# Performance work log

Hardware: AMD Instinct MI355X
Metric: run time of the kernel (lower is better)

The kernel has to match this reference:

```python
import jax, jax.numpy as jnp
import numpy as np
from jax import lax

EPS = 1e-5
NEG_SLOPE = 0.1
RES_SCALE = float(np.sqrt(0.5))


def upsample2x(x):
    # bilinear, align_corners=False (half-pixel), matches torch nn.Upsample(mode='bilinear')
    B, C, H, W = x.shape
    return jax.image.resize(x, (B, C, 2 * H, 2 * W), method='bilinear')


def modulated_conv2d(x, weight, styles, eps=EPS):
    # x: [B, I, H, W]; weight: [O, I, kh, kw]; styles: [B, I]
    B, I, H, W = x.shape
    O, _, kh, kw = weight.shape
    wmod = weight[None] * styles[:, None, :, None, None]            # [B,O,I,kh,kw]
    demod = lax.rsqrt(jnp.sum(wmod * wmod, axis=(2, 3, 4)) + eps)   # [B,O]
    wmod = wmod * demod[:, :, None, None, None]
    x_g = x.reshape(1, B * I, H, W)
    w_g = wmod.reshape(B * O, I, kh, kw)
    out = lax.conv_general_dilated(
        x_g, w_g, window_strides=(1, 1), padding=[(1, 1), (1, 1)],
        feature_group_count=B,
        dimension_numbers=('NCHW', 'OIHW', 'NCHW'))
    return out.reshape(B, O, H, W)


def style_block(x, w, n, conv_w, A_w, A_b, B_w, B_b, upsample):
    if upsample:
        x = upsample2x(x)
    scores = w @ A_w.T + A_b                      # [B, in_ch]
    x = modulated_conv2d(x, conv_w, scores)
    noise = n @ B_w.T + B_b                        # [B, out_ch]
    x = x + noise[:, :, None, None]
    return jnp.where(x >= 0, x, NEG_SLOPE * x)     # LeakyReLU(0.1)


def setup_inputs() -> dict:
    key = jax.random.key(0)
    ks = jax.random.split(key, 16)
    Bn, Ci, Co, Wd, Nd, H = 8, 256, 128, 512, 512, 64
    s = lambda k, shape, scale=0.05: jax.random.normal(k, shape, jnp.float32) * scale
    return {
        'x': jax.random.normal(ks[0], (Bn, Ci, H, H), jnp.float32),
        'w': jax.random.normal(ks[1], (Bn, Wd), jnp.float32),
        'n': jax.random.normal(ks[2], (Bn, Nd), jnp.float32),
        'rgb': jax.random.normal(ks[3], (Bn, 3, H, H), jnp.float32),
        'conv1_w': s(ks[4], (Ci, Ci, 3, 3)),
        'A1_w': s(ks[5], (Ci, Wd)), 'A1_b': jnp.ones((Ci,), jnp.float32),
        'B1_w': s(ks[6], (Ci, Nd)), 'B1_b': jnp.zeros((Ci,), jnp.float32),
        'conv2_w': s(ks[7], (Co, Ci, 3, 3)),
        'A2_w': s(ks[8], (Ci, Wd)), 'A2_b': jnp.ones((Ci,), jnp.float32),
        'B2_w': s(ks[9], (Co, Nd)), 'B2_b': jnp.zeros((Co,), jnp.float32),
        'rgb_w': s(ks[10], (3, Co, 1, 1)),
        'rgb_b': jnp.zeros((3,), jnp.float32),
    }


def reference(x, w, n, rgb, conv1_w, A1_w, A1_b, B1_w, B1_b,
              conv2_w, A2_w, A2_b, B2_w, B2_b, rgb_w, rgb_b):
    x = style_block(x, w, n, conv1_w, A1_w, A1_b, B1_w, B1_b, upsample=False)
    x = style_block(x, w, n, conv2_w, A2_w, A2_b, B2_w, B2_b, upsample=True)
    to_rgb = lax.conv_general_dilated(
        x, rgb_w, (1, 1), padding=[(0, 0), (0, 0)],
        dimension_numbers=('NCHW', 'OIHW', 'NCHW')) + rgb_b[None, :, None, None]
    rgb_out = (to_rgb + upsample2x(rgb)) * RES_SCALE
    return x, rgb_out
```

## Files before the change

### kernel.cpp

```cpp
#include <hip/hip_runtime.h>
#include <math.h>

#define BN 8
#define C1 256
#define C2 128
#define WD 512

typedef float  f32x4  __attribute__((ext_vector_type(4)));
typedef short  bf16x8 __attribute__((ext_vector_type(8)));
typedef unsigned short ushort_t;
typedef ushort_t us8 __attribute__((ext_vector_type(8)));
typedef ushort_t us4 __attribute__((ext_vector_type(4)));

__device__ __forceinline__ int clampi(int v, int lo, int hi) {
    return v < lo ? lo : (v > hi ? hi : v);
}
__device__ __forceinline__ float bf2f(ushort_t u) {
    return __uint_as_float(((unsigned int)u) << 16);
}
__device__ __forceinline__ ushort_t f2bf(float f) {
    unsigned int u = __float_as_uint(f);
    u = (u + 0x7fff + ((u >> 16) & 1)) >> 16;
    return (ushort_t)u;
}

__global__ __launch_bounds__(256)
void affine_kernel(const float* __restrict__ w, const float* __restrict__ n,
                   const float* __restrict__ A1w, const float* __restrict__ A1b,
                   const float* __restrict__ B1w, const float* __restrict__ B1b,
                   const float* __restrict__ A2w, const float* __restrict__ A2b,
                   const float* __restrict__ B2w, const float* __restrict__ B2b,
                   float* __restrict__ s1, float* __restrict__ s2,
                   float* __restrict__ n1, float* __restrict__ n2) {
    int tid = threadIdx.x;
    int gw = blockIdx.x * 4 + (tid >> 6);
    int lane = tid & 63;
    if (gw >= BN * 896) return;
    int b = gw / 896;
    int j = gw % 896;
    const float* vec; const float* M; const float* bias; float* out; int o;
    if (j < 256)      { o = j;       vec = w + b * WD; M = A1w; bias = A1b; out = s1 + b * 256; }
    else if (j < 512) { o = j - 256; vec = w + b * WD; M = A2w; bias = A2b; out = s2 + b * 256; }
    else if (j < 768) { o = j - 512; vec = n + b * WD; M = B1w; bias = B1b; out = n1 + b * 256; }
    else              { o = j - 768; vec = n + b * WD; M = B2w; bias = B2b; out = n2 + b * 128; }
    const float* row = M + (size_t)o * WD;
    int k0 = lane * 8;
    float4 v0 = *(const float4*)(vec + k0), v1 = *(const float4*)(vec + k0 + 4);
    float4 r0 = *(const float4*)(row + k0), r1 = *(const float4*)(row + k0 + 4);
    float acc = v0.x*r0.x + v0.y*r0.y + v0.z*r0.z + v0.w*r0.w
              + v1.x*r1.x + v1.y*r1.y + v1.z*r1.z + v1.w*r1.w;
    #pragma unroll
    for (int m = 1; m < 64; m <<= 1) acc += __shfl_xor(acc, m, 64);
    if (lane == 0) out[o] = acc + bias[o];
}

__global__ __launch_bounds__(256)
void demod_kernel(const float* __restrict__ cw1, const float* __restrict__ cw2,
                  const float* __restrict__ s1, const float* __restrict__ s2,
                  float* __restrict__ d1, float* __restrict__ d2) {
    int tid = threadIdx.x;
    int gw = blockIdx.x * 4 + (tid >> 6);
    int lane = tid & 63;
    if (gw >= BN * 384) return;
    int b = gw / 384;
    int j = gw % 384;
    const float* wbase; const float* s; float* dout; int o;
    if (j < 256) { o = j;       wbase = cw1; s = s1 + b * 256; dout = d1 + b * 256; }
    else         { o = j - 256; wbase = cw2; s = s2 + b * 256; dout = d2 + b * 128; }
    float acc = 0.f;
    #pragma unroll
    for (int i = 0; i < 4; i++) {
        int ic = lane * 4 + i;
        float sv = s[ic]; sv *= sv;
        const float* wk = wbase + ((size_t)o * 256 + ic) * 9;
        float t = 0.f;
        #pragma unroll
        for (int k = 0; k < 9; k++) t += wk[k] * wk[k];
        acc += t * sv;
    }
    #pragma unroll
    for (int m = 1; m < 64; m <<= 1) acc += __shfl_xor(acc, m, 64);
    if (lane == 0) dout[o] = rsqrtf(acc + 1e-5f);
}

__global__ __launch_bounds__(256)
void wprep_kernel(const float* __restrict__ cw1, const float* __restrict__ cw2,
                  ushort_t* __restrict__ wT1, ushort_t* __restrict__ wT2) {
    int idx = blockIdx.x * 256 + threadIdx.x;
    if (idx < 256 * 256) {
        int oc = idx >> 8, ic = idx & 255;
        int kc = ic >> 5, icw = ic & 31;
        const float* src = cw1 + ((size_t)(oc * 256 + ic)) * 9;
        #pragma unroll
        for (int tap = 0; tap < 9; tap++)
            wT1[((size_t)((kc * 9 + tap) * 256 + oc)) * 32 + icw] = f2bf(src[tap]);
    } else if (idx < 256 * 256 + 128 * 256) {
        int e = idx - 256 * 256;
        int oc = e >> 8, ic = e & 255;
        int kc = ic >> 5, icw = ic & 31;
        const float* src = cw2 + ((size_t)(oc * 256 + ic)) * 9;
        #pragma unroll
        for (int tap = 0; tap < 9; tap++)
            wT2[((size_t)((kc * 9 + tap) * 128 + oc)) * 32 + icw] = f2bf(src[tap]);
    }
}

__global__ __launch_bounds__(256)
void xprep_kernel(const float* __restrict__ x, const float* __restrict__ s1,
                  ushort_t* __restrict__ xTp) {
    __shared__ ushort_t tile[64 * 264];
    int b = blockIdx.y;
    int px0 = blockIdx.x * 64;
    int t = threadIdx.x;
    int pxl = (t & 15) * 4;
    int icb = t >> 4;
    const float* xb = x + (((size_t)b * C1) << 12) + px0;
    #pragma unroll
    for (int p = 0; p < 16; p++) {
        int ic = p * 16 + icb;
        float sv = s1[b * 256 + ic];
        float4 v = *(const float4*)(xb + (((size_t)ic) << 12) + pxl);
        tile[(pxl + 0) * 264 + ic] = f2bf(v.x * sv);
        tile[(pxl + 1) * 264 + ic] = f2bf(v.y * sv);
        tile[(pxl + 2) * 264 + ic] = f2bf(v.z * sv);
        tile[(pxl + 3) * 264 + ic] = f2bf(v.w * sv);
    }
    __syncthreads();
    ushort_t* outb = xTp + ((size_t)b << 20) + (size_t)px0 * 256;
    #pragma unroll
    for (int p = 0; p < 8; p++) {
        int u = t + 256 * p;
        int px = u >> 5, w8 = u & 31;
        us8 v = *(const us8*)(tile + px * 264 + w8 * 8);
        *(us8*)(outb + (size_t)px * 256 + w8 * 8) = v;
    }
}

__global__ __launch_bounds__(256)
void upsample_kernel(const ushort_t* __restrict__ y1T, const float* __restrict__ s2,
                     ushort_t* __restrict__ y1up) {
    int flat = blockIdx.x * 256 + threadIdx.x;
    int b = blockIdx.y;
    int ic8 = flat & 31;
    int pxl = flat >> 5;
    int ux = pxl & 127, uy = pxl >> 7;
    int jyA; float wyA;
    if (uy & 1) { jyA = uy >> 1;       wyA = 0.75f; }
    else        { jyA = (uy >> 1) - 1; wyA = 0.25f; }
    int jxA; float wxA;
    if (ux & 1) { jxA = ux >> 1;       wxA = 0.75f; }
    else        { jxA = (ux >> 1) - 1; wxA = 0.25f; }
    int yA = clampi(jyA, 0, 63), yB = clampi(jyA + 1, 0, 63);
    int xA = clampi(jxA, 0, 63), xB = clampi(jxA + 1, 0, 63);
    float wyB = 1.f - wyA, wxB = 1.f - wxA;
    const ushort_t* yb = y1T + (((size_t)b) << 20) + ic8 * 8;
    us8 qAA = *(const us8*)(yb + (size_t)(yA * 64 + xA) * 256);
    us8 qAB = *(const us8*)(yb + (size_t)(yA * 64 + xB) * 256);
    us8 qBA = *(const us8*)(yb + (size_t)(yB * 64 + xA) * 256);
    us8 qBB = *(const us8*)(yb + (size_t)(yB * 64 + xB) * 256);
    float4 slo = *(const float4*)(s2 + b * 256 + ic8 * 8);
    float4 shi = *(const float4*)(s2 + b * 256 + ic8 * 8 + 4);
    float sv[8] = {slo.x, slo.y, slo.z, slo.w, shi.x, shi.y, shi.z, shi.w};
    us8 h;
    #pragma unroll
    for (int j = 0; j < 8; j++) {
        float v = wyA * (wxA * bf2f(qAA[j]) + wxB * bf2f(qAB[j]))
                + wyB * (wxA * bf2f(qBA[j]) + wxB * bf2f(qBB[j]));
        h[j] = f2bf(v * sv[j]);
    }
    *(us8*)(y1up + ((size_t)b << 22) + (size_t)(uy * 128 + ux) * 256 + ic8 * 8) = h;
}

template<int IW, int OCTOT, int TPR, bool IS_CONV2>
__global__ __launch_bounds__(256, 2)
void conv_mfma(const ushort_t* __restrict__ inp, const ushort_t* __restrict__ wT,
               const float* __restrict__ dmod, const float* __restrict__ nza,
               ushort_t* __restrict__ outT,
               const float* __restrict__ rgb_in, const float* __restrict__ rw,
               const float* __restrict__ rb, float* __restrict__ xout,
               float* __restrict__ rgbo) {
    __shared__ __align__(16) ushort_t smem[28928];
    ushort_t* actS = smem;
    ushort_t* wS   = smem + 10432;

    const int b = blockIdx.z, ocg = blockIdx.y, tile = blockIdx.x;
    const int tyT = tile / TPR, txT = tile % TPR;
    const int ty0 = tyT * 16, tx0 = txT * 16;
    const int tid = threadIdx.x, lane = tid & 63, wave = tid >> 6;
    const int col = lane & 15, quad = lane >> 4;

    const ushort_t* inb = inp + (size_t)b * IW * IW * 256;

    int actOff[6]; bool actOk[6];
    #pragma unroll
    for (int i = 0; i < 6; i++) {
        int u = tid + 256 * i;
        int px_l = u >> 2, q = u & 3;
        int py = px_l / 18, pxx = px_l - py * 18;
        int gy = ty0 + py - 1, gx = tx0 + pxx - 1;
        bool ok = (u < 1296) && (gy >= 0) && (gy < IW) && (gx >= 0) && (gx < IW);
        actOk[i] = ok;
        actOff[i] = ok ? ((gy * IW + gx) * 256 + q * 8) : 0;
    }
    int wOff[9];
    #pragma unroll
    for (int i = 0; i < 9; i++) {
        int u = tid + 256 * i;
        int tap = u >> 8, oc = (u >> 2) & 63, q = u & 3;
        wOff[i] = (tap * OCTOT + ocg * 64 + oc) * 32 + q * 8;
    }
    const int KSTRIDE = 9 * OCTOT * 32;

    us8 aReg[6], wReg[9];
    const us8 zer = (us8)0;
#define LOADK(KC) { \
    _Pragma("unroll") for (int i = 0; i < 6; i++) \
        aReg[i] = actOk[i] ? *(const us8*)(inb + actOff[i] + (KC) * 32) : zer; \
    _Pragma("unroll") for (int i = 0; i < 9; i++) \
        wReg[i] = *(const us8*)(wT + wOff[i] + (KC) * KSTRIDE); }
#define STOREK() { \
    _Pragma("unroll") for (int i = 0; i < 6; i++) { \
        int u = tid + 256 * i; \
        if (u < 1296) *(us8*)(actS + (u & 3) * 2608 + (u >> 2) * 8) = aReg[i]; } \
    _Pragma("unroll") for (int i = 0; i < 9; i++) { \
        int u = tid + 256 * i; \
        *(us8*)(wS + (u & 3) * 4624 + (u >> 2) * 8) = wReg[i]; } }

    f32x4 acc[4][4];
    #pragma unroll
    for (int mt = 0; mt < 4; mt++)
        #pragma unroll
        for (int nt = 0; nt < 4; nt++) acc[mt][nt] = (f32x4)(0.f);

    LOADK(0);
    STOREK();
    __syncthreads();

    const ushort_t* bbase = actS + quad * 2608 + (72 * wave + col) * 8;
    const ushort_t* abase = wS + quad * 4624 + col * 8;

    for (int kc = 0; kc < 8; kc++) {
        if (kc < 7) LOADK(kc + 1);
        #pragma unroll
        for (int dx = 0; dx < 3; dx++) {
            bf16x8 bb[6];
            #pragma unroll
            for (int r = 0; r < 6; r++)
                bb[r] = *(const bf16x8*)(bbase + (r * 18 + dx) * 8);
            #pragma unroll
            for (int dy = 0; dy < 3; dy++) {
                const int tap = dy * 3 + dx;
                bf16x8 a[4];
                #pragma unroll
                for (int mt = 0; mt < 4; mt++)
                    a[mt] = *(const bf16x8*)(abase + (tap * 64 + mt * 16) * 8);
                #pragma unroll
                for (int mt = 0; mt < 4; mt++)
                    #pragma unroll
                    for (int nt = 0; nt < 4; nt++)
                        acc[mt][nt] = __builtin_amdgcn_mfma_f32_16x16x32_bf16(
                            a[mt], bb[nt + dy], acc[mt][nt], 0, 0, 0);
            }
        }
        __syncthreads();
        if (kc < 7) { STOREK(); }
        __syncthreads();
    }
#undef LOADK
#undef STOREK

    if constexpr (!IS_CONV2) {
        ushort_t* oS = smem;
        #pragma unroll
        for (int mt = 0; mt < 4; mt++) {
            int oc0 = ocg * 64 + mt * 16 + quad * 4;
            float4 dv = *(const float4*)(dmod + b * OCTOT + oc0);
            float4 nv = *(const float4*)(nza + b * OCTOT + oc0);
            float dva[4] = {dv.x, dv.y, dv.z, dv.w};
            float nva[4] = {nv.x, nv.y, nv.z, nv.w};
            #pragma unroll
            for (int nt = 0; nt < 4; nt++) {
                int px = (4 * wave + nt) * 16 + col;
                us4 h;
                #pragma unroll
                for (int r = 0; r < 4; r++) {
                    float t = acc[mt][nt][r] * dva[r] + nva[r];
                    t = (t >= 0.f) ? t : 0.1f * t;
                    h[r] = f2bf(t);
                }
                *(us4*)(oS + px * 80 + mt * 16 + quad * 4) = h;
            }
        }
        __syncthreads();
        #pragma unroll
        for (int p = 0; p < 8; p++) {
            int idx = tid + 256 * p;
            int px = idx >> 3, oc8 = idx & 7;
            us8 v = *(const us8*)(oS + px * 80 + oc8 * 8);
            int gy = ty0 + (px >> 4), gx = tx0 + (px & 15);
            *(us8*)(outT + ((size_t)b * IW * IW + gy * IW + gx) * 256 + ocg * 64 + oc8 * 8) = v;
        }
    } else {
        float dva[4][4], nva[4][4], rwa[3][4][4];
        #pragma unroll
        for (int mt = 0; mt < 4; mt++) {
            int oc0 = ocg * 64 + mt * 16 + quad * 4;
            float4 dv = *(const float4*)(dmod + b * 128 + oc0);
            float4 nv = *(const float4*)(nza + b * 128 + oc0);
            dva[mt][0] = dv.x; dva[mt][1] = dv.y; dva[mt][2] = dv.z; dva[mt][3] = dv.w;
            nva[mt][0] = nv.x; nva[mt][1] = nv.y; nva[mt][2] = nv.z; nva[mt][3] = nv.w;
            #pragma unroll
            for (int c = 0; c < 3; c++) {
                float4 rv = *(const float4*)(rw + c * 128 + oc0);
                rwa[c][mt][0] = rv.x; rwa[c][mt][1] = rv.y; rwa[c][mt][2] = rv.z; rwa[c][mt][3] = rv.w;
            }
        }
        #pragma unroll
        for (int nt = 0; nt < 4; nt++) {
            int uy = ty0 + 4 * wave + nt, ux = tx0 + col;
            float pc0 = 0.f, pc1 = 0.f, pc2 = 0.f;
            #pragma unroll
            for (int mt = 0; mt < 4; mt++) {
                int oc0 = ocg * 64 + mt * 16 + quad * 4;
                #pragma unroll
                for (int r = 0; r < 4; r++) {
                    float t = acc[mt][nt][r] * dva[mt][r] + nva[mt][r];
                    t = (t >= 0.f) ? t : 0.1f * t;
                    xout[(((size_t)b * 128 + oc0 + r) << 14) + (uy << 7) + ux] = t;
                    pc0 += rwa[0][mt][r] * t;
                    pc1 += rwa[1][mt][r] * t;
                    pc2 += rwa[2][mt][r] * t;
                }
            }
            pc0 += __shfl_xor(pc0, 16, 64); pc0 += __shfl_xor(pc0, 32, 64);
            pc1 += __shfl_xor(pc1, 16, 64); pc1 += __shfl_xor(pc1, 32, 64);
            pc2 += __shfl_xor(pc2, 16, 64); pc2 += __shfl_xor(pc2, 32, 64);
            if (quad == 0) {
                if (ocg == 0) {
                    int jyA; float wyA;
                    if (uy & 1) { jyA = uy >> 1;       wyA = 0.75f; }
                    else        { jyA = (uy >> 1) - 1; wyA = 0.25f; }
                    int jxA; float wxA;
                    if (ux & 1) { jxA = ux >> 1;       wxA = 0.75f; }
                    else        { jxA = (ux >> 1) - 1; wxA = 0.25f; }
                    int yA = clampi(jyA, 0, 63), yB = clampi(jyA + 1, 0, 63);
                    int xA = clampi(jxA, 0, 63), xB = clampi(jxA + 1, 0, 63);
                    float wyB = 1.f - wyA, wxB = 1.f - wxA;
                    const float* rp3 = rgb_in + (((size_t)b * 3) << 12);
                    #pragma unroll
                    for (int c = 0; c < 3; c++) {
                        const float* rc = rp3 + ((size_t)c << 12);
                        float up = wyA * (wxA * rc[(yA << 6) + xA] + wxB * rc[(yA << 6) + xB])
                                 + wyB * (wxA * rc[(yB << 6) + xA] + wxB * rc[(yB << 6) + xB]);
                        if (c == 0) pc0 += rb[0] + up;
                        else if (c == 1) pc1 += rb[1] + up;
                        else pc2 += rb[2] + up;
                    }
                }
                const float S = 0.70710678118654752f;
                atomicAdd(rgbo + (((size_t)b * 3 + 0) << 14) + (uy << 7) + ux, pc0 * S);
                atomicAdd(rgbo + (((size_t)b * 3 + 1) << 14) + (uy << 7) + ux, pc1 * S);
                atomicAdd(rgbo + (((size_t)b * 3 + 2) << 14) + (uy << 7) + ux, pc2 * S);
            }
        }
    }
}

extern "C" void kernel_launch(void* const* d_in, const int* in_sizes, int n_in,
                              void* d_out, int out_size, void* d_ws, size_t ws_size,
                              hipStream_t stream) {
    (void)in_sizes; (void)n_in; (void)out_size; (void)ws_size;
    const float* x     = (const float*)d_in[0];
    const float* w     = (const float*)d_in[1];
    const float* n     = (const float*)d_in[2];
    const float* rgb   = (const float*)d_in[3];
    const float* cw1   = (const float*)d_in[4];
    const float* A1w   = (const float*)d_in[5];
    const float* A1b   = (const float*)d_in[6];
    const float* B1w   = (const float*)d_in[7];
    const float* B1b   = (const float*)d_in[8];
    const float* cw2   = (const float*)d_in[9];
    const float* A2w   = (const float*)d_in[10];
    const float* A2b   = (const float*)d_in[11];
    const float* B2w   = (const float*)d_in[12];
    const float* B2b   = (const float*)d_in[13];
    const float* rgbw  = (const float*)d_in[14];
    const float* rgbb  = (const float*)d_in[15];

    char* ws = (char*)d_ws;
    float* s1 = (float*)(ws);
    float* s2 = (float*)(ws + 8192);
    float* d1 = (float*)(ws + 16384);
    float* d2 = (float*)(ws + 24576);
    float* n1 = (float*)(ws + 28672);
    float* n2 = (float*)(ws + 36864);
    ushort_t* wT1  = (ushort_t*)(ws + 40960);
    ushort_t* wT2  = (ushort_t*)(ws + 1220608);
    ushort_t* xTp  = (ushort_t*)(ws + 1810432);
    ushort_t* y1up = (ushort_t*)(ws + 18587648);
    ushort_t* y1T  = (ushort_t*)(ws + 85696512);

    float* xout = (float*)d_out;
    float* rgbo = xout + (size_t)BN * C2 * 128 * 128;

    hipMemsetAsync(rgbo, 0, (size_t)BN * 3 * 128 * 128 * 4, stream);

    affine_kernel<<<1792, 256, 0, stream>>>(w, n, A1w, A1b, B1w, B1b, A2w, A2b, B2w, B2b,
                                            s1, s2, n1, n2);
    demod_kernel<<<768, 256, 0, stream>>>(cw1, cw2, s1, s2, d1, d2);
    wprep_kernel<<<(256 * 256 + 128 * 256) / 256, 256, 0, stream>>>(cw1, cw2, wT1, wT2);
    xprep_kernel<<<dim3(64, BN), 256, 0, stream>>>(x, s1, xTp);
    conv_mfma<64, 256, 4, false><<<dim3(16, 4, BN), 256, 0, stream>>>(
        xTp, wT1, d1, n1, y1T, nullptr, nullptr, nullptr, nullptr, nullptr);
    upsample_kernel<<<dim3(2048, BN), 256, 0, stream>>>(y1T, s2, y1up);
    conv_mfma<128, 128, 8, true><<<dim3(64, 2, BN), 256, 0, stream>>>(
        y1up, wT2, d2, n2, nullptr, rgb, rgbw, rgbb, xout, rgbo);
}
```

Baseline: 262.8 us.

## Fuse bilinear upsample into conv2 activation load and fold style into per-batch weights

Removes the standalone upsample kernel and its large intermediate buffer. Conv2 now gathers four bf16 neighbours from the low-resolution activation for each staged pixel and interpolates them on the fly. The style scaling s2 moves from the activations into per-batch bf16 copies of the conv2 weights built in wprep. This saves a full write and read of the 128x128x256 upsampled tensor, at the cost of four times as many global loads and extra ALU work in conv2's load stage, plus eight times more weight-prep work and weight traffic.

```diff
diff --git a/kernel.cpp b/kernel.cpp
--- a/kernel.cpp
+++ b/kernel.cpp
@@ -85,7 +85,8 @@
 
 __global__ __launch_bounds__(256)
 void wprep_kernel(const float* __restrict__ cw1, const float* __restrict__ cw2,
-                  ushort_t* __restrict__ wT1, ushort_t* __restrict__ wT2) {
+                  const float* __restrict__ s2,
+                  ushort_t* __restrict__ wT1, ushort_t* __restrict__ wT2b) {
     int idx = blockIdx.x * 256 + threadIdx.x;
     if (idx < 256 * 256) {
         int oc = idx >> 8, ic = idx & 255;
@@ -94,14 +95,18 @@
         #pragma unroll
         for (int tap = 0; tap < 9; tap++)
             wT1[((size_t)((kc * 9 + tap) * 256 + oc)) * 32 + icw] = f2bf(src[tap]);
-    } else if (idx < 256 * 256 + 128 * 256) {
+    } else if (idx < 256 * 256 + BN * 128 * 256) {
         int e = idx - 256 * 256;
-        int oc = e >> 8, ic = e & 255;
+        int b = e >> 15;
+        int r = e & 32767;
+        int oc = r >> 8, ic = r & 255;
         int kc = ic >> 5, icw = ic & 31;
         const float* src = cw2 + ((size_t)(oc * 256 + ic)) * 9;
+        float sv = s2[b * 256 + ic];
+        ushort_t* dst = wT2b + (size_t)b * 294912;
         #pragma unroll
         for (int tap = 0; tap < 9; tap++)
-            wT2[((size_t)((kc * 9 + tap) * 128 + oc)) * 32 + icw] = f2bf(src[tap]);
+            dst[((size_t)((kc * 9 + tap) * 128 + oc)) * 32 + icw] = f2bf(src[tap] * sv);
     }
 }
 
@@ -134,41 +139,6 @@
         us8 v = *(const us8*)(tile + px * 264 + w8 * 8);
         *(us8*)(outb + (size_t)px * 256 + w8 * 8) = v;
     }
-}
-
-__global__ __launch_bounds__(256)
-void upsample_kernel(const ushort_t* __restrict__ y1T, const float* __restrict__ s2,
-                     ushort_t* __restrict__ y1up) {
-    int flat = blockIdx.x * 256 + threadIdx.x;
-    int b = blockIdx.y;
-    int ic8 = flat & 31;
-    int pxl = flat >> 5;
-    int ux = pxl & 127, uy = pxl >> 7;
-    int jyA; float wyA;
-    if (uy & 1) { jyA = uy >> 1;       wyA = 0.75f; }
-    else        { jyA = (uy >> 1) - 1; wyA = 0.25f; }
-    int jxA; float wxA;
-    if (ux & 1) { jxA = ux >> 1;       wxA = 0.75f; }
-    else        { jxA = (ux >> 1) - 1; wxA = 0.25f; }
-    int yA = clampi(jyA, 0, 63), yB = clampi(jyA + 1, 0, 63);
-    int xA = clampi(jxA, 0, 63), xB = clampi(jxA + 1, 0, 63);
-    float wyB = 1.f - wyA, wxB = 1.f - wxA;
-    const ushort_t* yb = y1T + (((size_t)b) << 20) + ic8 * 8;
-    us8 qAA = *(const us8*)(yb + (size_t)(yA * 64 + xA) * 256);
-    us8 qAB = *(const us8*)(yb + (size_t)(yA * 64 + xB) * 256);
-    us8 qBA = *(const us8*)(yb + (size_t)(yB * 64 + xA) * 256);
-    us8 qBB = *(const us8*)(yb + (size_t)(yB * 64 + xB) * 256);
-    float4 slo = *(const float4*)(s2 + b * 256 + ic8 * 8);
-    float4 shi = *(const float4*)(s2 + b * 256 + ic8 * 8 + 4);
-    float sv[8] = {slo.x, slo.y, slo.z, slo.w, shi.x, shi.y, shi.z, shi.w};
-    us8 h;
-    #pragma unroll
-    for (int j = 0; j < 8; j++) {
-        float v = wyA * (wxA * bf2f(qAA[j]) + wxB * bf2f(qAB[j]))
-                + wyB * (wxA * bf2f(qBA[j]) + wxB * bf2f(qBB[j]));
-        h[j] = f2bf(v * sv[j]);
-    }
-    *(us8*)(y1up + ((size_t)b << 22) + (size_t)(uy * 128 + ux) * 256 + ic8 * 8) = h;
 }
 
 template<int IW, int OCTOT, int TPR, bool IS_CONV2>
@@ -189,9 +159,13 @@
     const int tid = threadIdx.x, lane = tid & 63, wave = tid >> 6;
     const int col = lane & 15, quad = lane >> 4;
 
-    const ushort_t* inb = inp + (size_t)b * IW * IW * 256;
+    const ushort_t* inb = IS_CONV2 ? (inp + ((size_t)b << 20))
+                                   : (inp + (size_t)b * IW * IW * 256);
+    const ushort_t* wTb = IS_CONV2 ? (wT + (size_t)b * 294912) : wT;
 
     int actOff[6]; bool actOk[6];
+    int oAA[6], oAB[6], oBA[6], oBB[6];
+    float wAA[6], wAB[6], wBA[6], wBB[6];
     #pragma unroll
     for (int i = 0; i < 6; i++) {
         int u = tid + 256 * i;
@@ -199,8 +173,28 @@
         int py = px_l / 18, pxx = px_l - py * 18;
         int gy = ty0 + py - 1, gx = tx0 + pxx - 1;
         bool ok = (u < 1296) && (gy >= 0) && (gy < IW) && (gx >= 0) && (gx < IW);
-        actOk[i] = ok;
-        actOff[i] = ok ? ((gy * IW + gx) * 256 + q * 8) : 0;
+        if constexpr (!IS_CONV2) {
+            actOk[i] = ok;
+            actOff[i] = ok ? ((gy * IW + gx) * 256 + q * 8) : 0;
+        } else {
+            int jyA; float wyA;
+            if (gy & 1) { jyA = gy >> 1;       wyA = 0.75f; }
+            else        { jyA = (gy >> 1) - 1; wyA = 0.25f; }
+            int jxA; float wxA;
+            if (gx & 1) { jxA = gx >> 1;       wxA = 0.75f; }
+            else        { jxA = (gx >> 1) - 1; wxA = 0.25f; }
+            int yA = clampi(jyA, 0, 63), yB = clampi(jyA + 1, 0, 63);
+            int xA = clampi(jxA, 0, 63), xB = clampi(jxA + 1, 0, 63);
+            float wyB = 1.f - wyA, wxB = 1.f - wxA;
+            oAA[i] = ok ? ((yA * 64 + xA) * 256 + q * 8) : 0;
+            oAB[i] = ok ? ((yA * 64 + xB) * 256 + q * 8) : 0;
+            oBA[i] = ok ? ((yB * 64 + xA) * 256 + q * 8) : 0;
+            oBB[i] = ok ? ((yB * 64 + xB) * 256 + q * 8) : 0;
+            wAA[i] = ok ? wyA * wxA : 0.f;
+            wAB[i] = ok ? wyA * wxB : 0.f;
+            wBA[i] = ok ? wyB * wxA : 0.f;
+            wBB[i] = ok ? wyB * wxB : 0.f;
+        }
     }
     int wOff[9];
     #pragma unroll
@@ -214,10 +208,26 @@
     us8 aReg[6], wReg[9];
     const us8 zer = (us8)0;
 #define LOADK(KC) { \
-    _Pragma("unroll") for (int i = 0; i < 6; i++) \
-        aReg[i] = actOk[i] ? *(const us8*)(inb + actOff[i] + (KC) * 32) : zer; \
+    if constexpr (!IS_CONV2) { \
+        _Pragma("unroll") for (int i = 0; i < 6; i++) \
+            aReg[i] = actOk[i] ? *(const us8*)(inb + actOff[i] + (KC) * 32) : zer; \
+    } else { \
+        _Pragma("unroll") for (int i = 0; i < 6; i++) { \
+            us8 vAA = *(const us8*)(inb + oAA[i] + (KC) * 32); \
+            us8 vAB = *(const us8*)(inb + oAB[i] + (KC) * 32); \
+            us8 vBA = *(const us8*)(inb + oBA[i] + (KC) * 32); \
+            us8 vBB = *(const us8*)(inb + oBB[i] + (KC) * 32); \
+            us8 h; \
+            _Pragma("unroll") for (int j = 0; j < 8; j++) { \
+                float v = wAA[i] * bf2f(vAA[j]) + wAB[i] * bf2f(vAB[j]) \
+                        + wBA[i] * bf2f(vBA[j]) + wBB[i] * bf2f(vBB[j]); \
+                h[j] = f2bf(v); \
+            } \
+            aReg[i] = h; \
+        } \
+    } \
     _Pragma("unroll") for (int i = 0; i < 9; i++) \
-        wReg[i] = *(const us8*)(wT + wOff[i] + (KC) * KSTRIDE); }
+        wReg[i] = *(const us8*)(wTb + wOff[i] + (KC) * KSTRIDE); }
 #define STOREK() { \
     _Pragma("unroll") for (int i = 0; i < 6; i++) { \
         int u = tid + 256 * i; \
@@ -395,10 +405,9 @@
     float* n1 = (float*)(ws + 28672);
     float* n2 = (float*)(ws + 36864);
     ushort_t* wT1  = (ushort_t*)(ws + 40960);
-    ushort_t* wT2  = (ushort_t*)(ws + 1220608);
-    ushort_t* xTp  = (ushort_t*)(ws + 1810432);
-    ushort_t* y1up = (ushort_t*)(ws + 18587648);
-    ushort_t* y1T  = (ushort_t*)(ws + 85696512);
+    ushort_t* wT2b = (ushort_t*)(ws + 1220608);
+    ushort_t* xTp  = (ushort_t*)(ws + 5939200);
+    ushort_t* y1T  = (ushort_t*)(ws + 22716416);
 
     float* xout = (float*)d_out;
     float* rgbo = xout + (size_t)BN * C2 * 128 * 128;
@@ -408,11 +417,10 @@
     affine_kernel<<<1792, 256, 0, stream>>>(w, n, A1w, A1b, B1w, B1b, A2w, A2b, B2w, B2b,
                                             s1, s2, n1, n2);
     demod_kernel<<<768, 256, 0, stream>>>(cw1, cw2, s1, s2, d1, d2);
-    wprep_kernel<<<(256 * 256 + 128 * 256) / 256, 256, 0, stream>>>(cw1, cw2, wT1, wT2);
+    wprep_kernel<<<(256 * 256 + BN * 128 * 256) / 256, 256, 0, stream>>>(cw1, cw2, s2, wT1, wT2b);
     xprep_kernel<<<dim3(64, BN), 256, 0, stream>>>(x, s1, xTp);
     conv_mfma<64, 256, 4, false><<<dim3(16, 4, BN), 256, 0, stream>>>(
         xTp, wT1, d1, n1, y1T, nullptr, nullptr, nullptr, nullptr, nullptr);
-    upsample_kernel<<<dim3(2048, BN), 256, 0, stream>>>(y1T, s2, y1up);
     conv_mfma<128, 128, 8, true><<<dim3(64, 2, BN), 256, 0, stream>>>(
-        y1up, wT2, d2, n2, nullptr, rgb, rgbw, rgbb, xout, rgbo);
-}
+        y1T, wT2b, d2, n2, nullptr, rgb, rgbw, rgbb, xout, rgbo);
+}
```

Result: slower. 351.9 us (+33.9%).
